# Kernel tuning notes

Hardware: AMD Instinct MI355X
Metric: run time of the kernel (lower is better)

Reference implementation:

```python
import jax, jax.numpy as jnp
import numpy as np

B, S, R, H = 256, 196, 1024, 512  # batch, att regions, rnn_size, att_hid_size


def setup_inputs() -> dict:
    key = jax.random.key(0)
    ks = jax.random.split(key, 8)
    return {
        "att_feats": jax.random.normal(ks[0], (B, S, R), dtype=jnp.float32),
        "p_att_feats": jax.random.normal(ks[1], (B, S, H), dtype=jnp.float32),
        "hidden": jax.random.normal(ks[2], (B, R), dtype=jnp.float32),
        "in_weights": jax.random.uniform(ks[3], (B, S), dtype=jnp.float32),
        "h2att_w": jax.random.normal(ks[4], (H, R), dtype=jnp.float32) * (1.0 / np.sqrt(R)),
        "h2att_b": jnp.full((H,), 0.1, dtype=jnp.float32),
        "alpha_w": jax.random.normal(ks[5], (1, H), dtype=jnp.float32) * (1.0 / np.sqrt(H)),
        "alpha_b": jnp.full((1,), 0.1, dtype=jnp.float32),
    }


def reference(att_feats, p_att_feats, hidden, in_weights, h2att_w, h2att_b, alpha_w, alpha_b):
    # att = in_weights * p_att_feats          [B, S, H]
    att = in_weights[:, :, None] * p_att_feats
    # att_h = h2att(hidden)                   [B, H] broadcast over S
    att_h = hidden @ h2att_w.T + h2att_b
    dot = jnp.tanh(att + att_h[:, None, :])   # [B, S, H]
    # alpha_net: Linear(H, 1) -> scores       [B, S]
    scores = jnp.einsum('bsh,h->bs', dot, alpha_w[0]) + alpha_b[0]
    weight = jax.nn.softmax(scores, axis=-1)  # [B, S]
    # weighted pooling: bmm(weight[:,None,:], att_feats).squeeze(1)
    att_res = jnp.einsum('bs,bsr->br', weight, att_feats)  # [B, R]
    return (att_res, weight)
```

## Files before the change

### kernel.cpp

```cpp
#include <hip/hip_runtime.h>
#include <math.h>

#define BN 256
#define SN 196
#define RN 1024
#define HN 512
#define KSPLIT 8
#define KCH 128

__device__ __forceinline__ float fast_tanh(float x) {
    float e = __expf(2.0f * x);
    return 1.0f - 2.0f * __builtin_amdgcn_rcpf(e + 1.0f);
}

__global__ __launch_bounds__(256) void k_gemm_partial(
    const float* __restrict__ hidden, const float* __restrict__ w,
    float* __restrict__ partial) {
    __shared__ float At[64][64];
    __shared__ float Bt[64][64];
    const int t  = threadIdx.x;
    const int b0 = blockIdx.x * 64;
    const int h0 = blockIdx.y * 64;
    const int kc = blockIdx.z;

    const int th4 = (t & 15) * 4;
    const int tb4 = (t >> 4) * 4;
    float4 acc0 = {0,0,0,0}, acc1 = {0,0,0,0}, acc2 = {0,0,0,0}, acc3 = {0,0,0,0};

    for (int sub = 0; sub < 2; ++sub) {
        const int k0 = kc * KCH + sub * 64;
        {
            const int row = t >> 2, kq = (t & 3) * 16;
            const float* srcA = hidden + (size_t)(b0 + row) * RN + k0 + kq;
            const float* srcB = w      + (size_t)(h0 + row) * RN + k0 + kq;
#pragma unroll
            for (int j = 0; j < 4; ++j) {
                float4 v = *(const float4*)(srcA + j * 4);
                int k = kq + j * 4;
                At[k][row] = v.x; At[k+1][row] = v.y; At[k+2][row] = v.z; At[k+3][row] = v.w;
            }
#pragma unroll
            for (int j = 0; j < 4; ++j) {
                float4 v = *(const float4*)(srcB + j * 4);
                int k = kq + j * 4;
                Bt[k][row] = v.x; Bt[k+1][row] = v.y; Bt[k+2][row] = v.z; Bt[k+3][row] = v.w;
            }
        }
        __syncthreads();
#pragma unroll 8
        for (int k = 0; k < 64; ++k) {
            float4 a  = *(const float4*)&At[k][tb4];
            float4 bb = *(const float4*)&Bt[k][th4];
            acc0.x = fmaf(a.x, bb.x, acc0.x); acc0.y = fmaf(a.x, bb.y, acc0.y);
            acc0.z = fmaf(a.x, bb.z, acc0.z); acc0.w = fmaf(a.x, bb.w, acc0.w);
            acc1.x = fmaf(a.y, bb.x, acc1.x); acc1.y = fmaf(a.y, bb.y, acc1.y);
            acc1.z = fmaf(a.y, bb.z, acc1.z); acc1.w = fmaf(a.y, bb.w, acc1.w);
            acc2.x = fmaf(a.z, bb.x, acc2.x); acc2.y = fmaf(a.z, bb.y, acc2.y);
            acc2.z = fmaf(a.z, bb.z, acc2.z); acc2.w = fmaf(a.z, bb.w, acc2.w);
            acc3.x = fmaf(a.w, bb.x, acc3.x); acc3.y = fmaf(a.w, bb.y, acc3.y);
            acc3.z = fmaf(a.w, bb.z, acc3.z); acc3.w = fmaf(a.w, bb.w, acc3.w);
        }
        __syncthreads();
    }
    float* dst = partial + ((size_t)kc * BN + b0 + tb4) * HN + h0 + th4;
    *(float4*)(dst)          = acc0;
    *(float4*)(dst + HN)     = acc1;
    *(float4*)(dst + 2 * HN) = acc2;
    *(float4*)(dst + 3 * HN) = acc3;
}

__global__ __launch_bounds__(1024) void k_fused(
    const float* __restrict__ partial, const float* __restrict__ bias,
    const float* __restrict__ p_att, const float* __restrict__ in_w,
    const float* __restrict__ alpha_w, const float* __restrict__ att_feats,
    float* __restrict__ att_res, float* __restrict__ weight_out) {
    __shared__ float att_h[HN];
    __shared__ float sc[256];
    __shared__ float red[16 * 256];
    const int b    = blockIdx.x;
    const int t    = threadIdx.x;
    const int wv   = t >> 6;
    const int lane = t & 63;

    if (t >= SN && t < 256) sc[t] = -1e30f;

    if (t < 128) {
        float4 s = *(const float4*)(bias + t * 4);
        const float* p = partial + (size_t)b * HN + t * 4;
#pragma unroll
        for (int kc = 0; kc < KSPLIT; ++kc) {
            float4 v = *(const float4*)(p + (size_t)kc * BN * HN);
            s.x += v.x; s.y += v.y; s.z += v.z; s.w += v.w;
        }
        *(float4*)&att_h[t * 4] = s;
    }
    __syncthreads();

    {
        const float4* a4 = (const float4*)alpha_w;
        float4 aw0 = a4[lane], aw1 = a4[lane + 64];
        float4 ah0 = *(const float4*)&att_h[lane * 4];
        float4 ah1 = *(const float4*)&att_h[(lane + 64) * 4];
        const float4* p4 = (const float4*)p_att;
        for (int si = wv; si < SN; si += 16) {
            float  iw = in_w[b * SN + si];
            size_t rb = (size_t)(b * SN + si) * (HN / 4);
            float4 p0 = p4[rb + lane];
            float4 p1 = p4[rb + lane + 64];
            float sum;
            sum  = fast_tanh(fmaf(iw, p0.x, ah0.x)) * aw0.x;
            sum += fast_tanh(fmaf(iw, p0.y, ah0.y)) * aw0.y;
            sum += fast_tanh(fmaf(iw, p0.z, ah0.z)) * aw0.z;
            sum += fast_tanh(fmaf(iw, p0.w, ah0.w)) * aw0.w;
            sum += fast_tanh(fmaf(iw, p1.x, ah1.x)) * aw1.x;
            sum += fast_tanh(fmaf(iw, p1.y, ah1.y)) * aw1.y;
            sum += fast_tanh(fmaf(iw, p1.z, ah1.z)) * aw1.z;
            sum += fast_tanh(fmaf(iw, p1.w, ah1.w)) * aw1.w;
#pragma unroll
            for (int off = 32; off; off >>= 1) sum += __shfl_xor(sum, off, 64);
            if (lane == 0) sc[si] = sum;
        }
    }
    __syncthreads();

    if (wv == 0) {
        float v0 = sc[lane], v1 = sc[lane + 64], v2 = sc[lane + 128], v3 = sc[lane + 192];
        float m = fmaxf(fmaxf(v0, v1), fmaxf(v2, v3));
#pragma unroll
        for (int off = 32; off; off >>= 1) m = fmaxf(m, __shfl_xor(m, off, 64));
        float e0 = __expf(v0 - m), e1 = __expf(v1 - m);
        float e2 = __expf(v2 - m), e3 = __expf(v3 - m);
        float s = e0 + e1 + e2 + e3;
#pragma unroll
        for (int off = 32; off; off >>= 1) s += __shfl_xor(s, off, 64);
        float inv = 1.0f / s;
        e0 *= inv; e1 *= inv; e2 *= inv; e3 *= inv;
        sc[lane] = e0; sc[lane + 64] = e1; sc[lane + 128] = e2; sc[lane + 192] = e3;
        float* wo = weight_out + (size_t)b * SN;
        wo[lane] = e0; wo[lane + 64] = e1; wo[lane + 128] = e2;
        if (lane + 192 < SN) wo[lane + 192] = e3;
    }
    __syncthreads();

    {
        const int g = wv >> 2, q = wv & 3;
        const float* base = att_feats + (size_t)b * SN * RN + q * 256 + lane * 4;
        float4 acc = {0,0,0,0};
        for (int i = 0; i < 49; i += 7) {
#pragma unroll
            for (int j = 0; j < 7; ++j) {
                int s = g + 4 * (i + j);
                float ws = sc[s];
                float4 v = *(const float4*)(base + (size_t)s * RN);
                acc.x = fmaf(ws, v.x, acc.x);
                acc.y = fmaf(ws, v.y, acc.y);
                acc.z = fmaf(ws, v.z, acc.z);
                acc.w = fmaf(ws, v.w, acc.w);
            }
        }
        *(float4*)&red[wv * 256 + lane * 4] = acc;
    }
    __syncthreads();
    {
        const int q2 = t >> 8, rr = t & 255;
        float r = red[q2 * 256 + rr] + red[(4 + q2) * 256 + rr]
                + red[(8 + q2) * 256 + rr] + red[(12 + q2) * 256 + rr];
        att_res[(size_t)b * RN + t] = r;
    }
}

extern "C" void kernel_launch(void* const* d_in, const int* in_sizes, int n_in,
                              void* d_out, int out_size, void* d_ws, size_t ws_size,
                              hipStream_t stream) {
    const float* att_feats   = (const float*)d_in[0];
    const float* p_att_feats = (const float*)d_in[1];
    const float* hidden      = (const float*)d_in[2];
    const float* in_weights  = (const float*)d_in[3];
    const float* h2att_w     = (const float*)d_in[4];
    const float* h2att_b     = (const float*)d_in[5];
    const float* alpha_w     = (const float*)d_in[6];

    float* att_res = (float*)d_out;
    float* weight  = (float*)d_out + BN * RN;
    float* partial = (float*)d_ws;

    k_gemm_partial<<<dim3(BN / 64, HN / 64, KSPLIT), 256, 0, stream>>>(hidden, h2att_w, partial);
    k_fused<<<BN, 1024, 0, stream>>>(partial, h2att_b, p_att_feats, in_weights,
                                     alpha_w, att_feats, att_res, weight);
}
```

Before: 362.2 us.

## Fuse h2att GEMV into attention kernel and prefetch p_att rows

Removes the separate split-K GEMM kernel and its workspace partial sums; each block now computes its batch row's att_h as a GEMV over the full h2att weight matrix, with hidden staged in shared memory. The first four p_att rows per wave are loaded into registers before the GEMV so their latency overlaps it. This saves a launch and the partial-sum round trip, but every block rereads the 2 MB weight matrix, relying on cache hits.

```diff
diff --git a/kernel.cpp b/kernel.cpp
--- a/kernel.cpp
+++ b/kernel.cpp
@@ -5,75 +5,19 @@
 #define SN 196
 #define RN 1024
 #define HN 512
-#define KSPLIT 8
-#define KCH 128
 
 __device__ __forceinline__ float fast_tanh(float x) {
     float e = __expf(2.0f * x);
     return 1.0f - 2.0f * __builtin_amdgcn_rcpf(e + 1.0f);
 }
 
-__global__ __launch_bounds__(256) void k_gemm_partial(
+__global__ __launch_bounds__(1024) void k_all(
     const float* __restrict__ hidden, const float* __restrict__ w,
-    float* __restrict__ partial) {
-    __shared__ float At[64][64];
-    __shared__ float Bt[64][64];
-    const int t  = threadIdx.x;
-    const int b0 = blockIdx.x * 64;
-    const int h0 = blockIdx.y * 64;
-    const int kc = blockIdx.z;
-
-    const int th4 = (t & 15) * 4;
-    const int tb4 = (t >> 4) * 4;
-    float4 acc0 = {0,0,0,0}, acc1 = {0,0,0,0}, acc2 = {0,0,0,0}, acc3 = {0,0,0,0};
-
-    for (int sub = 0; sub < 2; ++sub) {
-        const int k0 = kc * KCH + sub * 64;
-        {
-            const int row = t >> 2, kq = (t & 3) * 16;
-            const float* srcA = hidden + (size_t)(b0 + row) * RN + k0 + kq;
-            const float* srcB = w      + (size_t)(h0 + row) * RN + k0 + kq;
-#pragma unroll
-            for (int j = 0; j < 4; ++j) {
-                float4 v = *(const float4*)(srcA + j * 4);
-                int k = kq + j * 4;
-                At[k][row] = v.x; At[k+1][row] = v.y; At[k+2][row] = v.z; At[k+3][row] = v.w;
-            }
-#pragma unroll
-            for (int j = 0; j < 4; ++j) {
-                float4 v = *(const float4*)(srcB + j * 4);
-                int k = kq + j * 4;
-                Bt[k][row] = v.x; Bt[k+1][row] = v.y; Bt[k+2][row] = v.z; Bt[k+3][row] = v.w;
-            }
-        }
-        __syncthreads();
-#pragma unroll 8
-        for (int k = 0; k < 64; ++k) {
-            float4 a  = *(const float4*)&At[k][tb4];
-            float4 bb = *(const float4*)&Bt[k][th4];
-            acc0.x = fmaf(a.x, bb.x, acc0.x); acc0.y = fmaf(a.x, bb.y, acc0.y);
-            acc0.z = fmaf(a.x, bb.z, acc0.z); acc0.w = fmaf(a.x, bb.w, acc0.w);
-            acc1.x = fmaf(a.y, bb.x, acc1.x); acc1.y = fmaf(a.y, bb.y, acc1.y);
-            acc1.z = fmaf(a.y, bb.z, acc1.z); acc1.w = fmaf(a.y, bb.w, acc1.w);
-            acc2.x = fmaf(a.z, bb.x, acc2.x); acc2.y = fmaf(a.z, bb.y, acc2.y);
-            acc2.z = fmaf(a.z, bb.z, acc2.z); acc2.w = fmaf(a.z, bb.w, acc2.w);
-            acc3.x = fmaf(a.w, bb.x, acc3.x); acc3.y = fmaf(a.w, bb.y, acc3.y);
-            acc3.z = fmaf(a.w, bb.z, acc3.z); acc3.w = fmaf(a.w, bb.w, acc3.w);
-        }
-        __syncthreads();
-    }
-    float* dst = partial + ((size_t)kc * BN + b0 + tb4) * HN + h0 + th4;
-    *(float4*)(dst)          = acc0;
-    *(float4*)(dst + HN)     = acc1;
-    *(float4*)(dst + 2 * HN) = acc2;
-    *(float4*)(dst + 3 * HN) = acc3;
-}
-
-__global__ __launch_bounds__(1024) void k_fused(
-    const float* __restrict__ partial, const float* __restrict__ bias,
-    const float* __restrict__ p_att, const float* __restrict__ in_w,
-    const float* __restrict__ alpha_w, const float* __restrict__ att_feats,
+    const float* __restrict__ bias, const float* __restrict__ p_att,
+    const float* __restrict__ in_w, const float* __restrict__ alpha_w,
+    const float* __restrict__ att_feats,
     float* __restrict__ att_res, float* __restrict__ weight_out) {
+    __shared__ float4 hid4[RN / 4];
     __shared__ float att_h[HN];
     __shared__ float sc[256];
     __shared__ float red[16 * 256];
@@ -83,30 +27,92 @@
     const int lane = t & 63;
 
     if (t >= SN && t < 256) sc[t] = -1e30f;
+    if (t < 256) hid4[t] = ((const float4*)(hidden + (size_t)b * RN))[t];
+    __syncthreads();
 
-    if (t < 128) {
-        float4 s = *(const float4*)(bias + t * 4);
-        const float* p = partial + (size_t)b * HN + t * 4;
+    float4 pf0[4], pf1[4];
+    float  pfw[4];
+    {
+        const float4* p4 = (const float4*)p_att;
 #pragma unroll
-        for (int kc = 0; kc < KSPLIT; ++kc) {
-            float4 v = *(const float4*)(p + (size_t)kc * BN * HN);
-            s.x += v.x; s.y += v.y; s.z += v.z; s.w += v.w;
+        for (int j = 0; j < 4; ++j) {
+            const int si = wv + 16 * j;
+            pfw[j] = in_w[b * SN + si];
+            const size_t rb = (size_t)(b * SN + si) * (HN / 4);
+            pf0[j] = p4[rb + lane];
+            pf1[j] = p4[rb + lane + 64];
         }
-        *(float4*)&att_h[t * 4] = s;
+    }
+
+    {
+        const float4 x0 = hid4[lane],       x1 = hid4[lane + 64],
+                     x2 = hid4[lane + 128], x3 = hid4[lane + 192];
+        const int hbase = wv * 32;
+        for (int r = 0; r < 32; r += 2) {
+            const float4* wa = (const float4*)(w + (size_t)(hbase + r) * RN);
+            const float4* wb = (const float4*)(w + (size_t)(hbase + r + 1) * RN);
+            float4 a0 = wa[lane], a1 = wa[lane + 64],
+                   a2 = wa[lane + 128], a3 = wa[lane + 192];
+            float4 c0 = wb[lane], c1 = wb[lane + 64],
+                   c2 = wb[lane + 128], c3 = wb[lane + 192];
+            float da0 = a0.x * x0.x, da1 = a1.x * x1.x;
+            da0 = fmaf(a0.y, x0.y, da0); da1 = fmaf(a1.y, x1.y, da1);
+            da0 = fmaf(a0.z, x0.z, da0); da1 = fmaf(a1.z, x1.z, da1);
+            da0 = fmaf(a0.w, x0.w, da0); da1 = fmaf(a1.w, x1.w, da1);
+            da0 = fmaf(a2.x, x2.x, da0); da1 = fmaf(a3.x, x3.x, da1);
+            da0 = fmaf(a2.y, x2.y, da0); da1 = fmaf(a3.y, x3.y, da1);
+            da0 = fmaf(a2.z, x2.z, da0); da1 = fmaf(a3.z, x3.z, da1);
+            da0 = fmaf(a2.w, x2.w, da0); da1 = fmaf(a3.w, x3.w, da1);
+            float db0 = c0.x * x0.x, db1 = c1.x * x1.x;
+            db0 = fmaf(c0.y, x0.y, db0); db1 = fmaf(c1.y, x1.y, db1);
+            db0 = fmaf(c0.z, x0.z, db0); db1 = fmaf(c1.z, x1.z, db1);
+            db0 = fmaf(c0.w, x0.w, db0); db1 = fmaf(c1.w, x1.w, db1);
+            db0 = fmaf(c2.x, x2.x, db0); db1 = fmaf(c3.x, x3.x, db1);
+            db0 = fmaf(c2.y, x2.y, db0); db1 = fmaf(c3.y, x3.y, db1);
+            db0 = fmaf(c2.z, x2.z, db0); db1 = fmaf(c3.z, x3.z, db1);
+            db0 = fmaf(c2.w, x2.w, db0); db1 = fmaf(c3.w, x3.w, db1);
+            float da = da0 + da1, db = db0 + db1;
+#pragma unroll
+            for (int off = 32; off; off >>= 1) {
+                da += __shfl_xor(da, off, 64);
+                db += __shfl_xor(db, off, 64);
+            }
+            if (lane == 0) {
+                att_h[hbase + r]     = da + bias[hbase + r];
+                att_h[hbase + r + 1] = db + bias[hbase + r + 1];
+            }
+        }
     }
     __syncthreads();
 
     {
         const float4* a4 = (const float4*)alpha_w;
-        float4 aw0 = a4[lane], aw1 = a4[lane + 64];
-        float4 ah0 = *(const float4*)&att_h[lane * 4];
-        float4 ah1 = *(const float4*)&att_h[(lane + 64) * 4];
+        const float4 aw0 = a4[lane], aw1 = a4[lane + 64];
+        const float4 ah0 = *(const float4*)&att_h[lane * 4];
+        const float4 ah1 = *(const float4*)&att_h[(lane + 64) * 4];
+#pragma unroll
+        for (int j = 0; j < 4; ++j) {
+            const int si = wv + 16 * j;
+            const float iw = pfw[j];
+            float4 p0 = pf0[j], p1 = pf1[j];
+            float sum;
+            sum  = fast_tanh(fmaf(iw, p0.x, ah0.x)) * aw0.x;
+            sum += fast_tanh(fmaf(iw, p0.y, ah0.y)) * aw0.y;
+            sum += fast_tanh(fmaf(iw, p0.z, ah0.z)) * aw0.z;
+            sum += fast_tanh(fmaf(iw, p0.w, ah0.w)) * aw0.w;
+            sum += fast_tanh(fmaf(iw, p1.x, ah1.x)) * aw1.x;
+            sum += fast_tanh(fmaf(iw, p1.y, ah1.y)) * aw1.y;
+            sum += fast_tanh(fmaf(iw, p1.z, ah1.z)) * aw1.z;
+            sum += fast_tanh(fmaf(iw, p1.w, ah1.w)) * aw1.w;
+#pragma unroll
+            for (int off = 32; off; off >>= 1) sum += __shfl_xor(sum, off, 64);
+            if (lane == 0) sc[si] = sum;
+        }
         const float4* p4 = (const float4*)p_att;
-        for (int si = wv; si < SN; si += 16) {
-            float  iw = in_w[b * SN + si];
-            size_t rb = (size_t)(b * SN + si) * (HN / 4);
-            float4 p0 = p4[rb + lane];
-            float4 p1 = p4[rb + lane + 64];
+        for (int si = wv + 64; si < SN; si += 16) {
+            const float iw = in_w[b * SN + si];
+            const size_t rb = (size_t)(b * SN + si) * (HN / 4);
+            float4 p0 = p4[rb + lane], p1 = p4[rb + lane + 64];
             float sum;
             sum  = fast_tanh(fmaf(iw, p0.x, ah0.x)) * aw0.x;
             sum += fast_tanh(fmaf(iw, p0.y, ah0.y)) * aw0.y;
@@ -145,7 +151,7 @@
     {
         const int g = wv >> 2, q = wv & 3;
         const float* base = att_feats + (size_t)b * SN * RN + q * 256 + lane * 4;
-        float4 acc = {0,0,0,0};
+        float4 acc = {0, 0, 0, 0};
         for (int i = 0; i < 49; i += 7) {
 #pragma unroll
             for (int j = 0; j < 7; ++j) {
@@ -182,9 +188,8 @@
 
     float* att_res = (float*)d_out;
     float* weight  = (float*)d_out + BN * RN;
-    float* partial = (float*)d_ws;
+    (void)d_ws; (void)ws_size;
 
-    k_gemm_partial<<<dim3(BN / 64, HN / 64, KSPLIT), 256, 0, stream>>>(hidden, h2att_w, partial);
-    k_fused<<<BN, 1024, 0, stream>>>(partial, h2att_b, p_att_feats, in_weights,
-                                     alpha_w, att_feats, att_res, weight);
+    k_all<<<BN, 1024, 0, stream>>>(hidden, h2att_w, h2att_b, p_att_feats,
+                                   in_weights, alpha_w, att_feats, att_res, weight);
 }
```

Result: slower. 379.2 us (+4.7%).

## Split fused attention kernel into scores, split-S pooling, and reduce kernels

Applied to the files above, without the earlier changes.

The single per-batch fused kernel is split into a scores/softmax kernel and a separate pooling kernel launched over (batch, 8 S-chunks) with 256 threads, followed by a reduction kernel over the partial sums. This raises the number of independent blocks streaming att_feats so more memory parallelism is exposed. The scores loop also processes two rows per wave iteration to increase loads in flight. The cost is two extra launches, a round trip of the weights through global memory, and an extra partial buffer of 8x256x1024 floats that is written and read back.

```diff
diff --git a/kernel.cpp b/kernel.cpp
--- a/kernel.cpp
+++ b/kernel.cpp
@@ -7,6 +7,7 @@
 #define HN 512
 #define KSPLIT 8
 #define KCH 128
+#define PSPLIT 8
 
 __device__ __forceinline__ float fast_tanh(float x) {
     float e = __expf(2.0f * x);
@@ -69,14 +70,12 @@
     *(float4*)(dst + 3 * HN) = acc3;
 }
 
-__global__ __launch_bounds__(1024) void k_fused(
+__global__ __launch_bounds__(1024) void k_scores(
     const float* __restrict__ partial, const float* __restrict__ bias,
     const float* __restrict__ p_att, const float* __restrict__ in_w,
-    const float* __restrict__ alpha_w, const float* __restrict__ att_feats,
-    float* __restrict__ att_res, float* __restrict__ weight_out) {
+    const float* __restrict__ alpha_w, float* __restrict__ weight_out) {
     __shared__ float att_h[HN];
     __shared__ float sc[256];
-    __shared__ float red[16 * 256];
     const int b    = blockIdx.x;
     const int t    = threadIdx.x;
     const int wv   = t >> 6;
@@ -98,27 +97,45 @@
 
     {
         const float4* a4 = (const float4*)alpha_w;
-        float4 aw0 = a4[lane], aw1 = a4[lane + 64];
-        float4 ah0 = *(const float4*)&att_h[lane * 4];
-        float4 ah1 = *(const float4*)&att_h[(lane + 64) * 4];
+        const float4 aw0 = a4[lane], aw1 = a4[lane + 64];
+        const float4 ah0 = *(const float4*)&att_h[lane * 4];
+        const float4 ah1 = *(const float4*)&att_h[(lane + 64) * 4];
         const float4* p4 = (const float4*)p_att;
-        for (int si = wv; si < SN; si += 16) {
-            float  iw = in_w[b * SN + si];
-            size_t rb = (size_t)(b * SN + si) * (HN / 4);
-            float4 p0 = p4[rb + lane];
-            float4 p1 = p4[rb + lane + 64];
-            float sum;
-            sum  = fast_tanh(fmaf(iw, p0.x, ah0.x)) * aw0.x;
-            sum += fast_tanh(fmaf(iw, p0.y, ah0.y)) * aw0.y;
-            sum += fast_tanh(fmaf(iw, p0.z, ah0.z)) * aw0.z;
-            sum += fast_tanh(fmaf(iw, p0.w, ah0.w)) * aw0.w;
-            sum += fast_tanh(fmaf(iw, p1.x, ah1.x)) * aw1.x;
-            sum += fast_tanh(fmaf(iw, p1.y, ah1.y)) * aw1.y;
-            sum += fast_tanh(fmaf(iw, p1.z, ah1.z)) * aw1.z;
-            sum += fast_tanh(fmaf(iw, p1.w, ah1.w)) * aw1.w;
-#pragma unroll
-            for (int off = 32; off; off >>= 1) sum += __shfl_xor(sum, off, 64);
-            if (lane == 0) sc[si] = sum;
+        for (int si = wv; si < SN; si += 32) {
+            const int  sj = si + 16;
+            const bool h2 = (sj < SN);
+            const float iw0 = in_w[b * SN + si];
+            const float iw1 = h2 ? in_w[b * SN + sj] : 0.0f;
+            const size_t r0 = (size_t)(b * SN + si) * (HN / 4);
+            const size_t r1 = (size_t)(b * SN + (h2 ? sj : si)) * (HN / 4);
+            float4 x00 = p4[r0 + lane], x01 = p4[r0 + lane + 64];
+            float4 x10 = p4[r1 + lane], x11 = p4[r1 + lane + 64];
+            float s0, s1;
+            s0  = fast_tanh(fmaf(iw0, x00.x, ah0.x)) * aw0.x;
+            s1  = fast_tanh(fmaf(iw1, x10.x, ah0.x)) * aw0.x;
+            s0 += fast_tanh(fmaf(iw0, x00.y, ah0.y)) * aw0.y;
+            s1 += fast_tanh(fmaf(iw1, x10.y, ah0.y)) * aw0.y;
+            s0 += fast_tanh(fmaf(iw0, x00.z, ah0.z)) * aw0.z;
+            s1 += fast_tanh(fmaf(iw1, x10.z, ah0.z)) * aw0.z;
+            s0 += fast_tanh(fmaf(iw0, x00.w, ah0.w)) * aw0.w;
+            s1 += fast_tanh(fmaf(iw1, x10.w, ah0.w)) * aw0.w;
+            s0 += fast_tanh(fmaf(iw0, x01.x, ah1.x)) * aw1.x;
+            s1 += fast_tanh(fmaf(iw1, x11.x, ah1.x)) * aw1.x;
+            s0 += fast_tanh(fmaf(iw0, x01.y, ah1.y)) * aw1.y;
+            s1 += fast_tanh(fmaf(iw1, x11.y, ah1.y)) * aw1.y;
+            s0 += fast_tanh(fmaf(iw0, x01.z, ah1.z)) * aw1.z;
+            s1 += fast_tanh(fmaf(iw1, x11.z, ah1.z)) * aw1.z;
+            s0 += fast_tanh(fmaf(iw0, x01.w, ah1.w)) * aw1.w;
+            s1 += fast_tanh(fmaf(iw1, x11.w, ah1.w)) * aw1.w;
+#pragma unroll
+            for (int off = 32; off; off >>= 1) {
+                s0 += __shfl_xor(s0, off, 64);
+                s1 += __shfl_xor(s1, off, 64);
+            }
+            if (lane == 0) {
+                sc[si] = s0;
+                if (h2) sc[sj] = s1;
+            }
         }
     }
     __syncthreads();
@@ -135,38 +152,59 @@
         for (int off = 32; off; off >>= 1) s += __shfl_xor(s, off, 64);
         float inv = 1.0f / s;
         e0 *= inv; e1 *= inv; e2 *= inv; e3 *= inv;
-        sc[lane] = e0; sc[lane + 64] = e1; sc[lane + 128] = e2; sc[lane + 192] = e3;
         float* wo = weight_out + (size_t)b * SN;
         wo[lane] = e0; wo[lane + 64] = e1; wo[lane + 128] = e2;
         if (lane + 192 < SN) wo[lane + 192] = e3;
     }
+}
+
+__global__ __launch_bounds__(256) void k_pool(
+    const float* __restrict__ weight, const float* __restrict__ att_feats,
+    float* __restrict__ pool_part) {
+    __shared__ float wsm[32];
+    const int b  = blockIdx.x, sq = blockIdx.y;
+    const int t  = threadIdx.x, q = t >> 6, lane = t & 63;
+    const int base = sq * 24 + (sq < 4 ? sq : 4);
+    const int cnt  = 24 + (sq < 4 ? 1 : 0);
+    if (t < cnt) wsm[t] = weight[b * SN + base + t];
     __syncthreads();
 
-    {
-        const int g = wv >> 2, q = wv & 3;
-        const float* base = att_feats + (size_t)b * SN * RN + q * 256 + lane * 4;
-        float4 acc = {0,0,0,0};
-        for (int i = 0; i < 49; i += 7) {
-#pragma unroll
-            for (int j = 0; j < 7; ++j) {
-                int s = g + 4 * (i + j);
-                float ws = sc[s];
-                float4 v = *(const float4*)(base + (size_t)s * RN);
-                acc.x = fmaf(ws, v.x, acc.x);
-                acc.y = fmaf(ws, v.y, acc.y);
-                acc.z = fmaf(ws, v.z, acc.z);
-                acc.w = fmaf(ws, v.w, acc.w);
-            }
-        }
-        *(float4*)&red[wv * 256 + lane * 4] = acc;
-    }
-    __syncthreads();
-    {
-        const int q2 = t >> 8, rr = t & 255;
-        float r = red[q2 * 256 + rr] + red[(4 + q2) * 256 + rr]
-                + red[(8 + q2) * 256 + rr] + red[(12 + q2) * 256 + rr];
-        att_res[(size_t)b * RN + t] = r;
-    }
+    const float* src = att_feats + (size_t)b * SN * RN + (size_t)base * RN
+                     + q * 256 + lane * 4;
+    float4 acc = {0, 0, 0, 0};
+    int i = 0;
+    for (; i + 5 <= cnt; i += 5) {
+#pragma unroll
+        for (int j = 0; j < 5; ++j) {
+            float ws = wsm[i + j];
+            float4 v = *(const float4*)(src + (size_t)(i + j) * RN);
+            acc.x = fmaf(ws, v.x, acc.x);
+            acc.y = fmaf(ws, v.y, acc.y);
+            acc.z = fmaf(ws, v.z, acc.z);
+            acc.w = fmaf(ws, v.w, acc.w);
+        }
+    }
+#pragma unroll
+    for (; i < cnt; ++i) {
+        float ws = wsm[i];
+        float4 v = *(const float4*)(src + (size_t)i * RN);
+        acc.x = fmaf(ws, v.x, acc.x);
+        acc.y = fmaf(ws, v.y, acc.y);
+        acc.z = fmaf(ws, v.z, acc.z);
+        acc.w = fmaf(ws, v.w, acc.w);
+    }
+    float* dst = pool_part + ((size_t)sq * BN + b) * RN + q * 256 + lane * 4;
+    *(float4*)dst = acc;
+}
+
+__global__ __launch_bounds__(256) void k_reduce(
+    const float* __restrict__ pool_part, float* __restrict__ att_res) {
+    const int e = blockIdx.x * 256 + threadIdx.x;
+    float s = 0.0f;
+#pragma unroll
+    for (int sq = 0; sq < PSPLIT; ++sq)
+        s += pool_part[(size_t)sq * BN * RN + e];
+    att_res[e] = s;
 }
 
 extern "C" void kernel_launch(void* const* d_in, const int* in_sizes, int n_in,
@@ -182,9 +220,13 @@
 
     float* att_res = (float*)d_out;
     float* weight  = (float*)d_out + BN * RN;
-    float* partial = (float*)d_ws;
-
-    k_gemm_partial<<<dim3(BN / 64, HN / 64, KSPLIT), 256, 0, stream>>>(hidden, h2att_w, partial);
-    k_fused<<<BN, 1024, 0, stream>>>(partial, h2att_b, p_att_feats, in_weights,
-                                     alpha_w, att_feats, att_res, weight);
-}
+    float* partial   = (float*)d_ws;
+    float* pool_part = (float*)d_ws + (size_t)KSPLIT * BN * HN;
+
+    k_gemm_partial<<<dim3(BN / 64, HN / 64, KSPLIT), 256, 0, stream>>>(
+        hidden, h2att_w, partial);
+    k_scores<<<BN, 1024, 0, stream>>>(partial, h2att_b, p_att_feats, in_weights,
+                                      alpha_w, weight);
+    k_pool<<<dim3(BN, PSPLIT), 256, 0, stream>>>(weight, att_feats, pool_part);
+    k_reduce<<<(BN * RN) / 256, 256, 0, stream>>>(pool_part, att_res);
+}
```

New measurement: 371.5 us. 2.6% more time.
